# Optimization experiments

Hardware: AMD Instinct MI355X
Metric: run time of the kernel (lower is better)

Reference implementation:

```python
import jax, jax.numpy as jnp
import numpy as np

B, S = 128, 256
BERT_DIM, HID, LATENT = 768, 512, 128
V = 4096        # size of valid-token id universe (valid_ids_set ~= arange(V))
K = 100         # n_clusters
VOCAB = 30522   # bow.shape[1]


def setup_inputs() -> dict:
    key = jax.random.key(0)
    ks = jax.random.split(key, 16)
    f = jnp.float32
    s = 0.02
    return {
        "input_ids": jax.random.randint(ks[0], (B, S), 0, V),
        "valid_pos": jnp.ones((B, S), jnp.int32),
        "attention_mask": jnp.ones((B, S), jnp.int32),
        "token_embs": jax.random.normal(ks[1], (B, S, BERT_DIM), f),
        "bow": jax.random.randint(ks[2], (B, VOCAB), 0, 2).astype(f),
        "enc_w1": jax.random.normal(ks[3], (BERT_DIM, HID), f) * s,
        "enc_b1": jnp.zeros((HID,), f),
        "enc_w2": jax.random.normal(ks[4], (HID, LATENT), f) * s,
        "enc_b2": jnp.zeros((LATENT,), f),
        "dec_w1": jax.random.normal(ks[5], (LATENT, HID), f) * s,
        "dec_b1": jnp.zeros((HID,), f),
        "dec_w2": jax.random.normal(ks[6], (HID, BERT_DIM), f) * s,
        "dec_b2": jnp.zeros((BERT_DIM,), f),
        "centers": jax.random.normal(ks[7], (K, LATENT), f),
        "counts": jnp.full((K,), 50.0, f),
        "vocab_weights": jax.random.uniform(ks[8], (VOCAB,), f),
    }


def reference(input_ids, valid_pos, attention_mask, token_embs, bow,
              enc_w1, enc_b1, enc_w2, enc_b2,
              dec_w1, dec_b1, dec_w2, dec_b2,
              centers, counts, vocab_weights):
    # valid_pos is all-ones -> valid_mask selects every token; flatten [B,S,D] -> [N,D]
    x = token_embs.reshape(-1, BERT_DIM)
    # AutoEncoder: encode, L2-normalize latent, decode
    h = jax.nn.relu(x @ enc_w1 + enc_b1)
    z = h @ enc_w2 + enc_b2
    z = z / jnp.linalg.norm(z, axis=-1, keepdims=True)          # latent_embs [N,LATENT]
    rec = jax.nn.relu(z @ dec_w1 + dec_b1) @ dec_w2 + dec_b2    # bert_embs_rec [N,768]
    # segment mean over unique token ids (valid_ids_set == arange(V))
    ids = input_ids.reshape(-1)
    seg_sum = jax.ops.segment_sum(z, ids, num_segments=V)
    freq = jax.ops.segment_sum(jnp.ones_like(ids, jnp.float32), ids, num_segments=V)
    avg = seg_sum / jnp.maximum(freq, 1.0)[:, None]             # avg_latent_embs [V,LATENT]
    # co-occurrence matrix: trans_matrix gathers bow columns at valid ids (= first V cols)
    nz = (bow[:, :V] != 0).astype(jnp.float32)                  # [B,V]
    p_i = nz.sum(axis=0) / B
    p_ij = (nz.T @ nz) / B                                      # [V,V]
    co_matrix = p_ij / p_i[:, None] / p_i[None, :]
    # soft k-means assignment: normalized centers, matmul, softmax, argmax
    cn = centers / jnp.linalg.norm(centers, axis=-1, keepdims=True)
    probs = jax.nn.softmax(avg @ cn.T, axis=-1)                 # [V,K]
    cluster_ids = jnp.argmax(probs, axis=1)
    # sequential EMA centroid update (equivalent ordering to per-cluster python loops;
    # clusters are independent so a single scan in sample order matches the original)
    w = vocab_weights[:V]
    valid = (freq > 0).astype(jnp.float32)                      # skip ids never seen

    def step(carry, inp):
        c, cnt = carry
        xi, ki, wi, vi = inp
        new_cnt = cnt[ki] + vi
        cnt = cnt.at[ki].set(new_cnt)
        eta = jnp.where(vi > 0, wi / new_cnt, 0.0)
        c = c.at[ki].set((1.0 - eta) * c[ki] + eta * xi)
        return (c, cnt), None

    (new_centers, _), _ = jax.lax.scan(step, (centers, counts), (avg, cluster_ids, w, valid))
    return co_matrix, rec, avg, cluster_ids, new_centers
```

## Files before the change

### kernel.cpp

```cpp
#include <hip/hip_runtime.h>
#include <cstdint>

#define M_TOK 32768
#define BERT  768
#define HID   512
#define LAT   128
#define NV    4096
#define NK    100
#define VOCAB 30522
#define NB    128

typedef short short8 __attribute__((ext_vector_type(8)));
typedef float floatx4 __attribute__((ext_vector_type(4)));
typedef int   intx4  __attribute__((ext_vector_type(4)));
typedef unsigned short u16x4 __attribute__((ext_vector_type(4)));

__device__ __forceinline__ unsigned short f2bf(float f) {
    unsigned u = __float_as_uint(f);
    unsigned r = (u + 0x7FFFu + ((u >> 16) & 1u)) >> 16;
    return (unsigned short)r;
}
__device__ __forceinline__ float bf2f(unsigned short h) {
    return __uint_as_float((unsigned)h << 16);
}

__device__ __forceinline__ void async16(const void* g, void* l) {
    __builtin_amdgcn_global_load_lds(
        (const __attribute__((address_space(1))) unsigned int*)g,
        (__attribute__((address_space(3))) unsigned int*)l, 16, 0, 0);
}

__global__ __launch_bounds__(256) void wsplit(
    const float* __restrict__ W, unsigned short* __restrict__ Wt,
    int K, int N)
{
    int j = blockIdx.x * 256 + threadIdx.x;
    int total = N * K;
    if (j >= total) return;
    int n = j / K, k = j - n * K;
    float v = W[(size_t)k * N + n];
    unsigned short h = f2bf(v);
    float r = v - bf2f(h);
    unsigned short m = f2bf(r);
    float r2 = r - bf2f(m);
    unsigned short l = f2bf(r2);
    Wt[j] = h;
    Wt[(size_t)total + j] = m;
    Wt[(size_t)2 * total + j] = l;
}

__global__ __launch_bounds__(256) void wsplit_i8(
    const float* __restrict__ W, signed char* __restrict__ Wt,
    int K, int N, float scale)
{
    int j = blockIdx.x * 256 + threadIdx.x;
    int total = N * K;
    if (j >= total) return;
    int n = j / K, k = j - n * K;
    float v = W[(size_t)k * N + n];
    int fx = (int)rintf(v * scale);
    fx = fx > 32639 ? 32639 : (fx < -32640 ? -32640 : fx);
    int b1 = ((fx + 128) & 255) - 128;
    int b0 = (fx - b1) >> 8;
    Wt[j] = (signed char)b0;
    Wt[(size_t)total + j] = (signed char)b1;
}

template<int NL, bool RELU, int OUT = 0>
__global__ __launch_bounds__(256) void gemm_mfma(
    const float* __restrict__ A, const unsigned short* __restrict__ Wt,
    const float* __restrict__ bias, float* __restrict__ C,
    int M, int N, int K)
{
    __shared__ unsigned short Ash[NL][128 * 32];
    __shared__ unsigned short Bsh[NL][128 * 32];

    const int tid  = threadIdx.x;
    const int lane = tid & 63;
    const int wave = tid >> 6;
    const int gx  = gridDim.x;
    const int id  = blockIdx.x + gx * blockIdx.y;
    const int bxp = (id >> 3) % gx;
    const int byp = (id & 7) + 8 * (id / (8 * gx));
    const int bm  = byp * 128;
    const int bn  = bxp * 128;
    const int wm = (wave & 1) * 64;
    const int wn = (wave >> 1) * 64;

    const int ar = tid >> 3;
    const int ak = (tid & 7) * 4;
    const int br = tid >> 2;
    const int bk = (tid & 3) * 8;

    floatx4 acc[4][4];
#pragma unroll
    for (int t = 0; t < 4; ++t)
#pragma unroll
        for (int u = 0; u < 4; ++u)
            acc[t][u] = (floatx4)0.0f;

    float4 av[4];
#pragma unroll
    for (int i = 0; i < 4; ++i)
        av[i] = *(const float4*)(A + (size_t)(bm + ar + 32 * i) * K + ak);

    for (int k0 = 0; k0 < K; k0 += 32) {
        u16x4 ah[NL][4];
#pragma unroll
        for (int i = 0; i < 4; ++i) {
            float vv[4] = {av[i].x, av[i].y, av[i].z, av[i].w};
#pragma unroll
            for (int e = 0; e < 4; ++e) {
                float v = vv[e];
                unsigned short h = f2bf(v);
                float r = v - bf2f(h);
                unsigned short m = f2bf(r);
                ah[0][i][e] = h;
                ah[1][i][e] = m;
                if constexpr (NL == 3) {
                    float r2 = r - bf2f(m);
                    ah[2][i][e] = f2bf(r2);
                }
            }
        }
        __syncthreads();
#pragma unroll
        for (int l = 0; l < NL; ++l) {
            const unsigned short* wp = Wt + (size_t)l * N * K;
#pragma unroll
            for (int i = 0; i < 2; ++i)
                async16(wp + (size_t)(bn + br + 64 * i) * K + k0 + bk,
                        &Bsh[l][i * 2048 + tid * 8]);
        }
#pragma unroll
        for (int l = 0; l < NL; ++l)
#pragma unroll
            for (int i = 0; i < 4; ++i)
                *(u16x4*)&Ash[l][(ar + 32 * i) * 32 + ak] = ah[l][i];
        if (k0 + 32 < K) {
#pragma unroll
            for (int i = 0; i < 4; ++i)
                av[i] = *(const float4*)(A + (size_t)(bm + ar + 32 * i) * K + k0 + 32 + ak);
        }
        __syncthreads();

        short8 af[NL][4];
#pragma unroll
        for (int l = 0; l < NL; ++l)
#pragma unroll
            for (int t = 0; t < 4; ++t)
                af[l][t] = *(const short8*)&Ash[l][(wm + t * 16 + (lane & 15)) * 32 + (lane >> 4) * 8];

#pragma unroll
        for (int bl = 0; bl < NL; ++bl) {
            short8 bf[4];
#pragma unroll
            for (int u = 0; u < 4; ++u)
                bf[u] = *(const short8*)&Bsh[bl][(wn + u * 16 + (lane & 15)) * 32 + (lane >> 4) * 8];
#pragma unroll
            for (int al = 0; al < NL; ++al) {
                if (al + bl >= NL) continue;
#pragma unroll
                for (int t = 0; t < 4; ++t)
#pragma unroll
                    for (int u = 0; u < 4; ++u)
                        acc[t][u] = __builtin_amdgcn_mfma_f32_16x16x32_bf16(
                            af[al][t], bf[u], acc[t][u], 0, 0, 0);
            }
        }
    }

    signed char* P0 = (signed char*)C;
    signed char* P1 = P0 + (size_t)M * N;
#pragma unroll
    for (int t = 0; t < 4; ++t) {
        int row0 = bm + wm + t * 16 + (lane >> 4) * 4;
#pragma unroll
        for (int u = 0; u < 4; ++u) {
            int col = bn + wn + u * 16 + (lane & 15);
            float b = bias[col];
#pragma unroll
            for (int r = 0; r < 4; ++r) {
                float v = acc[t][u][r] + b;
                if (RELU) v = fmaxf(v, 0.f);
                if constexpr (OUT == 0) {
                    C[(size_t)(row0 + r) * N + col] = v;
                } else {
                    int fx = (int)rintf(v * 65536.f);
                    fx = fx > 32639 ? 32639 : (fx < 0 ? 0 : fx);
                    int a1 = ((fx + 128) & 255) - 128;
                    int a0 = (fx - a1) >> 8;
                    P0[(size_t)(row0 + r) * N + col] = (signed char)a0;
                    P1[(size_t)(row0 + r) * N + col] = (signed char)a1;
                }
            }
        }
    }
}

__global__ __launch_bounds__(256) void gemm_i8(
    const signed char* __restrict__ Ap, const signed char* __restrict__ Bp,
    const float* __restrict__ bias, float* __restrict__ C,
    int M, int N, int K)
{
    __shared__ signed char Ash[2][128 * 64];
    __shared__ signed char Bsh[2][128 * 64];

    const int tid  = threadIdx.x;
    const int lane = tid & 63;
    const int wave = tid >> 6;
    const int gx  = gridDim.x;
    const int id  = blockIdx.x + gx * blockIdx.y;
    const int bxp = (id >> 3) % gx;
    const int byp = (id & 7) + 8 * (id / (8 * gx));
    const int bm  = byp * 128;
    const int bn  = bxp * 128;
    const int wm = (wave & 1) * 64;
    const int wn = (wave >> 1) * 64;

    const int laneR = lane & 15;
    const int kgrp  = lane >> 4;
    const int gsw   = (laneR + (laneR >> 2)) & 3;
    const int slotb = ((kgrp ^ gsw) << 4);

    const int srow = tid >> 2;
    const int sp   = tid & 3;

    intx4 acc0[4][4], acc1[4][4];
#pragma unroll
    for (int t = 0; t < 4; ++t)
#pragma unroll
        for (int u = 0; u < 4; ++u) {
            acc0[t][u] = (intx4)0;
            acc1[t][u] = (intx4)0;
        }

    for (int k0 = 0; k0 < K; k0 += 64) {
        __syncthreads();
#pragma unroll
        for (int l = 0; l < 2; ++l) {
            const signed char* pa = Ap + (size_t)l * M * K + k0;
            const signed char* pb = Bp + (size_t)l * N * K + k0;
#pragma unroll
            for (int i = 0; i < 2; ++i) {
                int row = srow + i * 64;
                int rg  = row & 15;
                int c   = sp ^ ((rg + (rg >> 2)) & 3);
                async16(pa + (size_t)(bm + row) * K + c * 16,
                        &Ash[l][row * 64 + sp * 16]);
                async16(pb + (size_t)(bn + row) * K + c * 16,
                        &Bsh[l][row * 64 + sp * 16]);
            }
        }
        __syncthreads();

        intx4 a[4][2], b[4][2];
#pragma unroll
        for (int l = 0; l < 2; ++l)
#pragma unroll
            for (int m = 0; m < 4; ++m) {
                a[m][l] = *(const intx4*)&Ash[l][(wm + m * 16 + laneR) * 64 + slotb];
                b[m][l] = *(const intx4*)&Bsh[l][(wn + m * 16 + laneR) * 64 + slotb];
            }

#pragma unroll
        for (int m = 0; m < 4; ++m)
#pragma unroll
            for (int u = 0; u < 4; ++u) {
                acc0[m][u] = __builtin_amdgcn_mfma_i32_16x16x64_i8(
                    a[m][0], b[u][0], acc0[m][u], 0, 0, 0);
                acc1[m][u] = __builtin_amdgcn_mfma_i32_16x16x64_i8(
                    a[m][1], b[u][0], acc1[m][u], 0, 0, 0);
                acc1[m][u] = __builtin_amdgcn_mfma_i32_16x16x64_i8(
                    a[m][0], b[u][1], acc1[m][u], 0, 0, 0);
            }
    }

#pragma unroll
    for (int t = 0; t < 4; ++t) {
        int row0 = bm + wm + t * 16 + (lane >> 4) * 4;
#pragma unroll
        for (int u = 0; u < 4; ++u) {
            int col = bn + wn + u * 16 + (lane & 15);
            float bb = bias[col];
#pragma unroll
            for (int r = 0; r < 4; ++r) {
                float v = (float)acc0[t][u][r] * 0x1p-18f
                        + (float)acc1[t][u][r] * 0x1p-26f + bb;
                C[(size_t)(row0 + r) * N + col] = v;
            }
        }
    }
}

__global__ __launch_bounds__(64) void rownorm128(const float* __restrict__ in,
                                                 float* __restrict__ out)
{
    int row = blockIdx.x;
    int l = threadIdx.x;
    const float* p = in + (size_t)row * 128;
    float v0 = p[l], v1 = p[l + 64];
    float s = v0 * v0 + v1 * v1;
#pragma unroll
    for (int o = 32; o > 0; o >>= 1) s += __shfl_xor(s, o, 64);
    float inv = 1.0f / sqrtf(s);
    float* q = out + (size_t)row * 128;
    q[l] = v0 * inv;
    q[l + 64] = v1 * inv;
}

__global__ __launch_bounds__(128) void seg_scatter(
    const float* __restrict__ z, const int* __restrict__ ids,
    float* __restrict__ seg, float* __restrict__ freq)
{
    int row = blockIdx.x;
    int l = threadIdx.x;
    int id = ids[row];
    atomicAdd(&seg[(size_t)id * 128 + l], z[(size_t)row * 128 + l]);
    if (l == 0) atomicAdd(&freq[id], 1.0f);
}

__global__ __launch_bounds__(128) void avg_kernel(
    const float* __restrict__ seg, const float* __restrict__ freq,
    float* __restrict__ avg)
{
    int i = blockIdx.x;
    int l = threadIdx.x;
    float f = fmaxf(freq[i], 1.0f);
    avg[(size_t)i * 128 + l] = seg[(size_t)i * 128 + l] / f;
}

__global__ __launch_bounds__(128) void argmax_kernel(
    const float* __restrict__ avg, const float* __restrict__ cn,
    int* __restrict__ cids, float* __restrict__ cids_f)
{
    __shared__ float arow[128];
    __shared__ float lg[NK];
    int row = blockIdx.x;
    int t = threadIdx.x;
    arow[t] = avg[(size_t)row * 128 + t];
    __syncthreads();
    if (t < NK) {
        float d = 0.f;
        const float* c = cn + (size_t)t * 128;
#pragma unroll 8
        for (int i = 0; i < 128; ++i) d += arow[i] * c[i];
        lg[t] = d;
    }
    __syncthreads();
    if (t == 0) {
        float best = lg[0];
        int bi = 0;
        for (int k = 1; k < NK; ++k) {
            if (lg[k] > best) { best = lg[k]; bi = k; }
        }
        cids[row] = bi;
        cids_f[row] = (float)bi;
    }
}

__global__ __launch_bounds__(256) void build_masks(
    const float* __restrict__ bow, unsigned long long* __restrict__ masks,
    float* __restrict__ cnt)
{
    int j = blockIdx.x * 256 + threadIdx.x;
    if (j >= NV) return;
    unsigned long long m0 = 0, m1 = 0;
    for (int b = 0; b < 64; ++b)
        if (bow[(size_t)b * VOCAB + j] != 0.f) m0 |= 1ull << b;
    for (int b = 0; b < 64; ++b)
        if (bow[(size_t)(b + 64) * VOCAB + j] != 0.f) m1 |= 1ull << b;
    masks[2 * j] = m0;
    masks[2 * j + 1] = m1;
    cnt[j] = (float)(__popcll(m0) + __popcll(m1));
}

__global__ __launch_bounds__(256) void co_kernel(
    const unsigned long long* __restrict__ masks, const float* __restrict__ cnt,
    float* __restrict__ co)
{
    int j = blockIdx.x * 256 + threadIdx.x;
    unsigned long long m0 = masks[2 * j], m1 = masks[2 * j + 1];
    float cj = cnt[j];
    int ibase = blockIdx.y * 64;
    for (int ii = 0; ii < 64; ++ii) {
        int i = ibase + ii;
        unsigned long long a0 = masks[2 * i], a1 = masks[2 * i + 1];
        float ci = cnt[i];
        float c = (float)(__popcll(a0 & m0) + __popcll(a1 & m1));
        co[(size_t)i * NV + j] = (float)NB * c / (ci * cj);
    }
}

__global__ __launch_bounds__(128) void cluster_scan(
    const float* __restrict__ avg, const int* __restrict__ cids,
    const float* __restrict__ freq, const float* __restrict__ vw,
    const float* __restrict__ centers, const float* __restrict__ counts,
    float* __restrict__ out_centers)
{
    __shared__ int list[NV];
    __shared__ float coef[NV];
    __shared__ int tcnt[128];
    __shared__ int tot;
    __shared__ float Ptot;

    int k = blockIdx.x;
    int t = threadIdx.x;

    int base = t * (NV / 128);
    int c = 0;
    for (int s = 0; s < NV / 128; ++s) {
        int i = base + s;
        if (cids[i] == k && freq[i] > 0.f) c++;
    }
    tcnt[t] = c;
    __syncthreads();
    if (t == 0) {
        int run = 0;
        for (int x = 0; x < 128; ++x) { int v = tcnt[x]; tcnt[x] = run; run += v; }
        tot = run;
    }
    __syncthreads();
    int off = tcnt[t];
    for (int s = 0; s < NV / 128; ++s) {
        int i = base + s;
        if (cids[i] == k && freq[i] > 0.f) list[off++] = i;
    }
    __syncthreads();
    int m = tot;

    float c0 = counts[k];
    for (int j = t; j < m; j += 128)
        coef[j] = vw[list[j]] / (c0 + (float)(j + 1));
    __syncthreads();
    if (t == 0) {
        float suf = 1.f;
        for (int j = m - 1; j >= 0; --j) {
            float e = coef[j];
            coef[j] = e * suf;
            suf *= (1.f - e);
        }
        Ptot = suf;
    }
    __syncthreads();

    float accv = Ptot * centers[(size_t)k * 128 + t];
    for (int j = 0; j < m; ++j)
        accv += coef[j] * avg[(size_t)list[j] * 128 + t];
    out_centers[(size_t)k * 128 + t] = accv;
}

__global__ __launch_bounds__(64) void cn_norm(const float* __restrict__ centers,
                                              float* __restrict__ cn)
{
    int row = blockIdx.x;
    int l = threadIdx.x;
    const float* p = centers + (size_t)row * 128;
    float v0 = p[l], v1 = p[l + 64];
    float s = v0 * v0 + v1 * v1;
#pragma unroll
    for (int o = 32; o > 0; o >>= 1) s += __shfl_xor(s, o, 64);
    float inv = 1.0f / sqrtf(s);
    cn[(size_t)row * 128 + l] = v0 * inv;
    cn[(size_t)row * 128 + l + 64] = v1 * inv;
}

extern "C" void kernel_launch(void* const* d_in, const int* in_sizes, int n_in,
                              void* d_out, int out_size, void* d_ws, size_t ws_size,
                              hipStream_t stream)
{
    const int*   input_ids = (const int*)d_in[0];
    const float* token_embs = (const float*)d_in[3];
    const float* bow       = (const float*)d_in[4];
    const float* enc_w1    = (const float*)d_in[5];
    const float* enc_b1    = (const float*)d_in[6];
    const float* enc_w2    = (const float*)d_in[7];
    const float* enc_b2    = (const float*)d_in[8];
    const float* dec_w1    = (const float*)d_in[9];
    const float* dec_b1    = (const float*)d_in[10];
    const float* dec_w2    = (const float*)d_in[11];
    const float* dec_b2    = (const float*)d_in[12];
    const float* centers   = (const float*)d_in[13];
    const float* counts    = (const float*)d_in[14];
    const float* vocab_w   = (const float*)d_in[15];

    float* out = (float*)d_out;
    const size_t OFF_CO  = 0;
    const size_t OFF_REC = 16777216;
    const size_t OFF_AVG = OFF_REC + 25165824;
    const size_t OFF_CID = OFF_AVG + 524288;
    const size_t OFF_NC  = OFF_CID + 4096;

    float* h    = (float*)d_ws;
    float* z    = h + (size_t)M_TOK * HID;
    float* seg  = z + (size_t)M_TOK * LAT;
    float* freq = seg + (size_t)NV * LAT;
    float* cn   = freq + NV;
    float* cntv = cn + (size_t)NK * LAT;
    int*   cids = (int*)(cntv + NV);
    unsigned long long* masks = (unsigned long long*)(cids + NV);
    unsigned short* wt1 = (unsigned short*)(masks + 2 * NV);
    unsigned short* wt2 = wt1 + (size_t)3 * HID * BERT;
    unsigned short* wt3 = wt2 + (size_t)3 * LAT * HID;
    signed char*    wi4 = (signed char*)(wt3 + (size_t)3 * HID * LAT);

    hipMemsetAsync(seg, 0, (size_t)(NV * LAT + NV) * sizeof(float), stream);

    wsplit<<<(BERT * HID + 255) / 256, 256, 0, stream>>>(enc_w1, wt1, BERT, HID);
    wsplit<<<(HID * LAT + 255) / 256, 256, 0, stream>>>(enc_w2, wt2, HID, LAT);
    wsplit<<<(LAT * HID + 255) / 256, 256, 0, stream>>>(dec_w1, wt3, LAT, HID);
    wsplit_i8<<<(HID * BERT + 255) / 256, 256, 0, stream>>>(
        dec_w2, wi4, HID, BERT, 262144.f);

    gemm_mfma<3, true ><<<dim3(HID / 128, M_TOK / 128), 256, 0, stream>>>(
        token_embs, wt1, enc_b1, h, M_TOK, HID, BERT);
    gemm_mfma<3, false><<<dim3(LAT / 128, M_TOK / 128), 256, 0, stream>>>(
        h, wt2, enc_b2, z, M_TOK, LAT, HID);
    rownorm128<<<M_TOK, 64, 0, stream>>>(z, z);

    gemm_mfma<2, true, 1><<<dim3(HID / 128, M_TOK / 128), 256, 0, stream>>>(
        z, wt3, dec_b1, h, M_TOK, HID, LAT);

    gemm_i8<<<dim3(BERT / 128, M_TOK / 128), 256, 0, stream>>>(
        (const signed char*)h, wi4, dec_b2, out + OFF_REC, M_TOK, BERT, HID);

    seg_scatter<<<M_TOK, 128, 0, stream>>>(z, input_ids, seg, freq);
    avg_kernel<<<NV, 128, 0, stream>>>(seg, freq, out + OFF_AVG);

    cn_norm<<<NK, 64, 0, stream>>>(centers, cn);
    argmax_kernel<<<NV, 128, 0, stream>>>(out + OFF_AVG, cn, cids, out + OFF_CID);

    build_masks<<<NV / 256, 256, 0, stream>>>(bow, masks, cntv);
    co_kernel<<<dim3(NV / 256, NV / 64), 256, 0, stream>>>(masks, cntv, out + OFF_CO);

    cluster_scan<<<NK, 128, 0, stream>>>(out + OFF_AVG, cids, freq, vocab_w,
                                         centers, counts, out + OFF_NC);
}
```

Measured before the change: 675.4 us.

## Replace bf16-split GEMMs with multi-limb int8 fixed-point MFMA GEMMs

The three remaining fp32-emulating GEMMs (encoder layers and the first decoder layer) switch from 3- or 2-way bf16 splitting to fixed-point int8 limb decomposition on the i8 MFMA path. Weights are pre-split into 3 or 2 signed int8 limbs, activations are quantized on the fly, and partial products are accumulated by limb order and recombined in float. Tiles shrink to 128x64 with a two-block occupancy hint. This uses the higher-throughput i8 MFMA with K=64 per instruction, but relies on fixed scales that could overflow or lose precision for inputs outside the expected range.

```diff
diff --git a/kernel.cpp b/kernel.cpp
--- a/kernel.cpp
+++ b/kernel.cpp
@@ -10,19 +10,8 @@
 #define VOCAB 30522
 #define NB    128
 
-typedef short short8 __attribute__((ext_vector_type(8)));
 typedef float floatx4 __attribute__((ext_vector_type(4)));
 typedef int   intx4  __attribute__((ext_vector_type(4)));
-typedef unsigned short u16x4 __attribute__((ext_vector_type(4)));
-
-__device__ __forceinline__ unsigned short f2bf(float f) {
-    unsigned u = __float_as_uint(f);
-    unsigned r = (u + 0x7FFFu + ((u >> 16) & 1u)) >> 16;
-    return (unsigned short)r;
-}
-__device__ __forceinline__ float bf2f(unsigned short h) {
-    return __uint_as_float((unsigned)h << 16);
-}
 
 __device__ __forceinline__ void async16(const void* g, void* l) {
     __builtin_amdgcn_global_load_lds(
@@ -30,24 +19,7 @@
         (__attribute__((address_space(3))) unsigned int*)l, 16, 0, 0);
 }
 
-__global__ __launch_bounds__(256) void wsplit(
-    const float* __restrict__ W, unsigned short* __restrict__ Wt,
-    int K, int N)
-{
-    int j = blockIdx.x * 256 + threadIdx.x;
-    int total = N * K;
-    if (j >= total) return;
-    int n = j / K, k = j - n * K;
-    float v = W[(size_t)k * N + n];
-    unsigned short h = f2bf(v);
-    float r = v - bf2f(h);
-    unsigned short m = f2bf(r);
-    float r2 = r - bf2f(m);
-    unsigned short l = f2bf(r2);
-    Wt[j] = h;
-    Wt[(size_t)total + j] = m;
-    Wt[(size_t)2 * total + j] = l;
-}
+__device__ __forceinline__ int swzg(int r) { return (r + (r >> 2)) & 3; }
 
 __global__ __launch_bounds__(256) void wsplit_i8(
     const float* __restrict__ W, signed char* __restrict__ Wt,
@@ -60,20 +32,203 @@
     float v = W[(size_t)k * N + n];
     int fx = (int)rintf(v * scale);
     fx = fx > 32639 ? 32639 : (fx < -32640 ? -32640 : fx);
-    int b1 = ((fx + 128) & 255) - 128;
+    int b1 = (int)(signed char)(fx & 255);
     int b0 = (fx - b1) >> 8;
     Wt[j] = (signed char)b0;
     Wt[(size_t)total + j] = (signed char)b1;
 }
 
-template<int NL, bool RELU, int OUT = 0>
-__global__ __launch_bounds__(256) void gemm_mfma(
-    const float* __restrict__ A, const unsigned short* __restrict__ Wt,
+__global__ __launch_bounds__(256) void wsplit_i8_3(
+    const float* __restrict__ W, signed char* __restrict__ Wt,
+    int K, int N, float scale)
+{
+    int j = blockIdx.x * 256 + threadIdx.x;
+    int total = N * K;
+    if (j >= total) return;
+    int n = j / K, k = j - n * K;
+    float v = W[(size_t)k * N + n];
+    int fx = (int)rintf(v * scale);
+    fx = fx > 8355711 ? 8355711 : (fx < -8355712 ? -8355712 : fx);
+    int b2 = (int)(signed char)(fx & 255);
+    int m  = (fx - b2) >> 8;
+    int b1 = (int)(signed char)(m & 255);
+    int b0 = (m - b1) >> 8;
+    Wt[j] = (signed char)b0;
+    Wt[(size_t)total + j] = (signed char)b1;
+    Wt[(size_t)2 * total + j] = (signed char)b2;
+}
+
+template<int NL, bool RELU, int OUT>
+__global__ __launch_bounds__(256, 2) void gemm_i8k(
+    const float* __restrict__ A, const signed char* __restrict__ Bt,
+    const float* __restrict__ bias, float* __restrict__ C,
+    int M, int N, int K, float ascale, float c0)
+{
+    __shared__ signed char Ash[NL][128 * 64];
+    __shared__ signed char Bsh[NL][64 * 64];
+
+    const int tid  = threadIdx.x;
+    const int lane = tid & 63;
+    const int wave = tid >> 6;
+    const int gx  = gridDim.x;
+    const int id  = blockIdx.x + gx * blockIdx.y;
+    const int bxp = (id >> 3) % gx;
+    const int byp = (id & 7) + 8 * (id / (8 * gx));
+    const int bm  = byp * 128;
+    const int bn  = bxp * 64;
+    const int wm  = (wave & 1) * 64;
+    const int wn  = (wave >> 1) * 32;
+
+    const int laneR = lane & 15;
+    const int kgrp  = lane >> 4;
+    const int slotb = ((kgrp ^ swzg(laneR)) << 4);
+
+    const int ar = tid >> 1;
+    const int sh = (tid & 1) * 8;
+    const int br = tid >> 2;
+    const int sp = tid & 3;
+    const int bcsw = sp ^ swzg(br & 15);
+
+    intx4 S0[4][2], S1[4][2], S2[4][2], S3[4][2];
+#pragma unroll
+    for (int m = 0; m < 4; ++m)
+#pragma unroll
+        for (int u = 0; u < 2; ++u) {
+            S0[m][u] = (intx4)0; S1[m][u] = (intx4)0;
+            if constexpr (NL == 3) { S2[m][u] = (intx4)0; S3[m][u] = (intx4)0; }
+        }
+
+    float4 av[8];
+#pragma unroll
+    for (int i = 0; i < 8; ++i)
+        av[i] = *(const float4*)(A + (size_t)(bm + ar) * K + (sh + i) * 4);
+
+    for (int k0 = 0; k0 < K; k0 += 64) {
+        unsigned pk[NL][8];
+#pragma unroll
+        for (int i = 0; i < 8; ++i) {
+            float vv[4] = {av[i].x, av[i].y, av[i].z, av[i].w};
+            unsigned p0 = 0, p1 = 0, p2 = 0;
+#pragma unroll
+            for (int e = 0; e < 4; ++e) {
+                int fx = (int)rintf(vv[e] * ascale);
+                if constexpr (NL == 3) {
+                    int lo  = (int)(signed char)(fx & 255);
+                    int m1  = (fx - lo) >> 8;
+                    int mid = (int)(signed char)(m1 & 255);
+                    int hi  = (m1 - mid) >> 8;
+                    p0 |= (unsigned)(hi  & 255) << (8 * e);
+                    p1 |= (unsigned)(mid & 255) << (8 * e);
+                    p2 |= (unsigned)(lo  & 255) << (8 * e);
+                } else {
+                    int lo = (int)(signed char)(fx & 255);
+                    int hi = (fx - lo) >> 8;
+                    p0 |= (unsigned)(hi & 255) << (8 * e);
+                    p1 |= (unsigned)(lo & 255) << (8 * e);
+                }
+            }
+            pk[0][i] = p0; pk[1][i] = p1;
+            if constexpr (NL == 3) pk[2][i] = p2;
+        }
+        __syncthreads();
+#pragma unroll
+        for (int l = 0; l < NL; ++l)
+            async16(Bt + (size_t)l * N * K + (size_t)(bn + br) * K + k0 + bcsw * 16,
+                    &Bsh[l][br * 64 + sp * 16]);
+        const int arg = swzg(ar & 15);
+#pragma unroll
+        for (int l = 0; l < NL; ++l)
+#pragma unroll
+            for (int i = 0; i < 8; ++i) {
+                int s = sh + i;
+                *(unsigned*)&Ash[l][ar * 64 + (((s >> 2) ^ arg) << 4) + (s & 3) * 4]
+                    = pk[l][i];
+            }
+        if (k0 + 64 < K) {
+#pragma unroll
+            for (int i = 0; i < 8; ++i)
+                av[i] = *(const float4*)(A + (size_t)(bm + ar) * K + k0 + 64 + (sh + i) * 4);
+        }
+        __syncthreads();
+
+        intx4 a[NL][4], b[NL][2];
+#pragma unroll
+        for (int l = 0; l < NL; ++l) {
+#pragma unroll
+            for (int m = 0; m < 4; ++m)
+                a[l][m] = *(const intx4*)&Ash[l][(wm + m * 16 + laneR) * 64 + slotb];
+#pragma unroll
+            for (int u = 0; u < 2; ++u)
+                b[l][u] = *(const intx4*)&Bsh[l][(wn + u * 16 + laneR) * 64 + slotb];
+        }
+
+#pragma unroll
+        for (int m = 0; m < 4; ++m)
+#pragma unroll
+            for (int u = 0; u < 2; ++u) {
+                S0[m][u] = __builtin_amdgcn_mfma_i32_16x16x64_i8(
+                    a[0][m], b[0][u], S0[m][u], 0, 0, 0);
+                S1[m][u] = __builtin_amdgcn_mfma_i32_16x16x64_i8(
+                    a[0][m], b[1][u], S1[m][u], 0, 0, 0);
+                S1[m][u] = __builtin_amdgcn_mfma_i32_16x16x64_i8(
+                    a[1][m], b[0][u], S1[m][u], 0, 0, 0);
+                if constexpr (NL == 3) {
+                    S2[m][u] = __builtin_amdgcn_mfma_i32_16x16x64_i8(
+                        a[0][m], b[2][u], S2[m][u], 0, 0, 0);
+                    S2[m][u] = __builtin_amdgcn_mfma_i32_16x16x64_i8(
+                        a[1][m], b[1][u], S2[m][u], 0, 0, 0);
+                    S2[m][u] = __builtin_amdgcn_mfma_i32_16x16x64_i8(
+                        a[2][m], b[0][u], S2[m][u], 0, 0, 0);
+                    S3[m][u] = __builtin_amdgcn_mfma_i32_16x16x64_i8(
+                        a[1][m], b[2][u], S3[m][u], 0, 0, 0);
+                    S3[m][u] = __builtin_amdgcn_mfma_i32_16x16x64_i8(
+                        a[2][m], b[1][u], S3[m][u], 0, 0, 0);
+                }
+            }
+    }
+
+    signed char* P0 = (signed char*)C;
+    signed char* P1 = P0 + (size_t)M * N;
+    const float h8 = 0x1p-8f;
+#pragma unroll
+    for (int m = 0; m < 4; ++m) {
+        int row0 = bm + wm + m * 16 + (lane >> 4) * 4;
+#pragma unroll
+        for (int u = 0; u < 2; ++u) {
+            int col = bn + wn + u * 16 + laneR;
+            float bb = bias[col];
+#pragma unroll
+            for (int r = 0; r < 4; ++r) {
+                float acc;
+                if constexpr (NL == 3)
+                    acc = (float)S0[m][u][r] + h8 * ((float)S1[m][u][r]
+                        + h8 * ((float)S2[m][u][r] + h8 * (float)S3[m][u][r]));
+                else
+                    acc = (float)S0[m][u][r] + h8 * (float)S1[m][u][r];
+                float v = c0 * acc + bb;
+                if (RELU) v = fmaxf(v, 0.f);
+                if constexpr (OUT == 0) {
+                    C[(size_t)(row0 + r) * N + col] = v;
+                } else {
+                    int fx = (int)rintf(v * 65536.f);
+                    fx = fx > 32639 ? 32639 : (fx < 0 ? 0 : fx);
+                    int a1 = (int)(signed char)(fx & 255);
+                    int a0 = (fx - a1) >> 8;
+                    P0[(size_t)(row0 + r) * N + col] = (signed char)a0;
+                    P1[(size_t)(row0 + r) * N + col] = (signed char)a1;
+                }
+            }
+        }
+    }
+}
+
+__global__ __launch_bounds__(256) void gemm_i8(
+    const signed char* __restrict__ Ap, const signed char* __restrict__ Bp,
     const float* __restrict__ bias, float* __restrict__ C,
     int M, int N, int K)
 {
-    __shared__ unsigned short Ash[NL][128 * 32];
-    __shared__ unsigned short Bsh[NL][128 * 32];
+    __shared__ signed char Ash[2][128 * 64];
+    __shared__ signed char Bsh[2][128 * 64];
 
     const int tid  = threadIdx.x;
     const int lane = tid & 63;
@@ -87,141 +242,9 @@
     const int wm = (wave & 1) * 64;
     const int wn = (wave >> 1) * 64;
 
-    const int ar = tid >> 3;
-    const int ak = (tid & 7) * 4;
-    const int br = tid >> 2;
-    const int bk = (tid & 3) * 8;
-
-    floatx4 acc[4][4];
-#pragma unroll
-    for (int t = 0; t < 4; ++t)
-#pragma unroll
-        for (int u = 0; u < 4; ++u)
-            acc[t][u] = (floatx4)0.0f;
-
-    float4 av[4];
-#pragma unroll
-    for (int i = 0; i < 4; ++i)
-        av[i] = *(const float4*)(A + (size_t)(bm + ar + 32 * i) * K + ak);
-
-    for (int k0 = 0; k0 < K; k0 += 32) {
-        u16x4 ah[NL][4];
-#pragma unroll
-        for (int i = 0; i < 4; ++i) {
-            float vv[4] = {av[i].x, av[i].y, av[i].z, av[i].w};
-#pragma unroll
-            for (int e = 0; e < 4; ++e) {
-                float v = vv[e];
-                unsigned short h = f2bf(v);
-                float r = v - bf2f(h);
-                unsigned short m = f2bf(r);
-                ah[0][i][e] = h;
-                ah[1][i][e] = m;
-                if constexpr (NL == 3) {
-                    float r2 = r - bf2f(m);
-                    ah[2][i][e] = f2bf(r2);
-                }
-            }
-        }
-        __syncthreads();
-#pragma unroll
-        for (int l = 0; l < NL; ++l) {
-            const unsigned short* wp = Wt + (size_t)l * N * K;
-#pragma unroll
-            for (int i = 0; i < 2; ++i)
-                async16(wp + (size_t)(bn + br + 64 * i) * K + k0 + bk,
-                        &Bsh[l][i * 2048 + tid * 8]);
-        }
-#pragma unroll
-        for (int l = 0; l < NL; ++l)
-#pragma unroll
-            for (int i = 0; i < 4; ++i)
-                *(u16x4*)&Ash[l][(ar + 32 * i) * 32 + ak] = ah[l][i];
-        if (k0 + 32 < K) {
-#pragma unroll
-            for (int i = 0; i < 4; ++i)
-                av[i] = *(const float4*)(A + (size_t)(bm + ar + 32 * i) * K + k0 + 32 + ak);
-        }
-        __syncthreads();
-
-        short8 af[NL][4];
-#pragma unroll
-        for (int l = 0; l < NL; ++l)
-#pragma unroll
-            for (int t = 0; t < 4; ++t)
-                af[l][t] = *(const short8*)&Ash[l][(wm + t * 16 + (lane & 15)) * 32 + (lane >> 4) * 8];
-
-#pragma unroll
-        for (int bl = 0; bl < NL; ++bl) {
-            short8 bf[4];
-#pragma unroll
-            for (int u = 0; u < 4; ++u)
-                bf[u] = *(const short8*)&Bsh[bl][(wn + u * 16 + (lane & 15)) * 32 + (lane >> 4) * 8];
-#pragma unroll
-            for (int al = 0; al < NL; ++al) {
-                if (al + bl >= NL) continue;
-#pragma unroll
-                for (int t = 0; t < 4; ++t)
-#pragma unroll
-                    for (int u = 0; u < 4; ++u)
-                        acc[t][u] = __builtin_amdgcn_mfma_f32_16x16x32_bf16(
-                            af[al][t], bf[u], acc[t][u], 0, 0, 0);
-            }
-        }
-    }
-
-    signed char* P0 = (signed char*)C;
-    signed char* P1 = P0 + (size_t)M * N;
-#pragma unroll
-    for (int t = 0; t < 4; ++t) {
-        int row0 = bm + wm + t * 16 + (lane >> 4) * 4;
-#pragma unroll
-        for (int u = 0; u < 4; ++u) {
-            int col = bn + wn + u * 16 + (lane & 15);
-            float b = bias[col];
-#pragma unroll
-            for (int r = 0; r < 4; ++r) {
-                float v = acc[t][u][r] + b;
-                if (RELU) v = fmaxf(v, 0.f);
-                if constexpr (OUT == 0) {
-                    C[(size_t)(row0 + r) * N + col] = v;
-                } else {
-                    int fx = (int)rintf(v * 65536.f);
-                    fx = fx > 32639 ? 32639 : (fx < 0 ? 0 : fx);
-                    int a1 = ((fx + 128) & 255) - 128;
-                    int a0 = (fx - a1) >> 8;
-                    P0[(size_t)(row0 + r) * N + col] = (signed char)a0;
-                    P1[(size_t)(row0 + r) * N + col] = (signed char)a1;
-                }
-            }
-        }
-    }
-}
-
-__global__ __launch_bounds__(256) void gemm_i8(
-    const signed char* __restrict__ Ap, const signed char* __restrict__ Bp,
-    const float* __restrict__ bias, float* __restrict__ C,
-    int M, int N, int K)
-{
-    __shared__ signed char Ash[2][128 * 64];
-    __shared__ signed char Bsh[2][128 * 64];
-
-    const int tid  = threadIdx.x;
-    const int lane = tid & 63;
-    const int wave = tid >> 6;
-    const int gx  = gridDim.x;
-    const int id  = blockIdx.x + gx * blockIdx.y;
-    const int bxp = (id >> 3) % gx;
-    const int byp = (id & 7) + 8 * (id / (8 * gx));
-    const int bm  = byp * 128;
-    const int bn  = bxp * 128;
-    const int wm = (wave & 1) * 64;
-    const int wn = (wave >> 1) * 64;
-
     const int laneR = lane & 15;
     const int kgrp  = lane >> 4;
-    const int gsw   = (laneR + (laneR >> 2)) & 3;
-    const int slotb = ((kgrp ^ gsw) << 4);
+    const int slotb = ((kgrp ^ swzg(laneR)) << 4);
 
     const int srow = tid >> 2;
     const int sp   = tid & 3;
@@ -244,8 +267,7 @@
 #pragma unroll
             for (int i = 0; i < 2; ++i) {
                 int row = srow + i * 64;
-                int rg  = row & 15;
-                int c   = sp ^ ((rg + (rg >> 2)) & 3);
+                int c   = sp ^ swzg(row & 15);
                 async16(pa + (size_t)(bm + row) * K + c * 16,
                         &Ash[l][row * 64 + sp * 16]);
                 async16(pb + (size_t)(bn + row) * K + c * 16,
@@ -499,27 +521,30 @@
     float* cntv = cn + (size_t)NK * LAT;
     int*   cids = (int*)(cntv + NV);
     unsigned long long* masks = (unsigned long long*)(cids + NV);
-    unsigned short* wt1 = (unsigned short*)(masks + 2 * NV);
-    unsigned short* wt2 = wt1 + (size_t)3 * HID * BERT;
-    unsigned short* wt3 = wt2 + (size_t)3 * LAT * HID;
-    signed char*    wi4 = (signed char*)(wt3 + (size_t)3 * HID * LAT);
+    signed char* wi1 = (signed char*)(masks + 2 * NV);
+    signed char* wi2 = wi1 + (size_t)3 * HID * BERT;
+    signed char* wi3 = wi2 + (size_t)3 * LAT * HID;
+    signed char* wi4 = wi3 + (size_t)2 * HID * LAT;
 
     hipMemsetAsync(seg, 0, (size_t)(NV * LAT + NV) * sizeof(float), stream);
 
-    wsplit<<<(BERT * HID + 255) / 256, 256, 0, stream>>>(enc_w1, wt1, BERT, HID);
-    wsplit<<<(HID * LAT + 255) / 256, 256, 0, stream>>>(enc_w2, wt2, HID, LAT);
-    wsplit<<<(LAT * HID + 255) / 256, 256, 0, stream>>>(dec_w1, wt3, LAT, HID);
+    wsplit_i8_3<<<(BERT * HID + 255) / 256, 256, 0, stream>>>(
+        enc_w1, wi1, BERT, HID, 67108864.f);
+    wsplit_i8_3<<<(HID * LAT + 255) / 256, 256, 0, stream>>>(
+        enc_w2, wi2, HID, LAT, 67108864.f);
+    wsplit_i8<<<(LAT * HID + 255) / 256, 256, 0, stream>>>(
+        dec_w1, wi3, LAT, HID, 262144.f);
     wsplit_i8<<<(HID * BERT + 255) / 256, 256, 0, stream>>>(
         dec_w2, wi4, HID, BERT, 262144.f);
 
-    gemm_mfma<3, true ><<<dim3(HID / 128, M_TOK / 128), 256, 0, stream>>>(
-        token_embs, wt1, enc_b1, h, M_TOK, HID, BERT);
-    gemm_mfma<3, false><<<dim3(LAT / 128, M_TOK / 128), 256, 0, stream>>>(
-        h, wt2, enc_b2, z, M_TOK, LAT, HID);
+    gemm_i8k<3, true, 0><<<dim3(HID / 64, M_TOK / 128), 256, 0, stream>>>(
+        token_embs, wi1, enc_b1, h, M_TOK, HID, BERT, 1048576.f, 0x1p-14f);
+    gemm_i8k<3, false, 0><<<dim3(LAT / 64, M_TOK / 128), 256, 0, stream>>>(
+        h, wi2, enc_b2, z, M_TOK, LAT, HID, 1048576.f, 0x1p-14f);
     rownorm128<<<M_TOK, 64, 0, stream>>>(z, z);
 
-    gemm_mfma<2, true, 1><<<dim3(HID / 128, M_TOK / 128), 256, 0, stream>>>(
-        z, wt3, dec_b1, h, M_TOK, HID, LAT);
+    gemm_i8k<2, true, 1><<<dim3(HID / 64, M_TOK / 128), 256, 0, stream>>>(
+        z, wi3, dec_b1, h, M_TOK, HID, LAT, 16384.f, 0x1p-16f);
 
     gemm_i8<<<dim3(BERT / 128, M_TOK / 128), 256, 0, stream>>>(
         (const signed char*)h, wi4, dec_b2, out + OFF_REC, M_TOK, BERT, HID);
```

Result: no change. 683.5 us (+1.2%).
